# Kernel tuning notes

Hardware: AMD Instinct MI355X
Metric: run time of the kernel (lower is better)

Reference implementation:

```python
import jax, jax.numpy as jnp
import numpy as np

NUM_RELATIONS = 65
NUM_GRAPHS = 1600


def rgcn_conv(x, src, dst, etype, W, Wroot, b):
    """PyG RGCNConv: per-relation mean aggregation + root transform + bias.
    out_i = x_i @ Wroot + b + sum_r mean_{j in N_r(i)} (x_j) @ W_r
    (mean-then-transform == transform-then-mean since W_r is linear).
    """
    N = x.shape[0]
    x_src = x[src]  # [E, in]
    etype_f = etype

    def body(acc, rW):
        r, Wr = rW
        m = (etype_f == r).astype(x.dtype)[:, None]  # [E,1]
        s = jax.ops.segment_sum(x_src * m, dst, num_segments=N)   # [N,in]
        cnt = jax.ops.segment_sum(m, dst, num_segments=N)          # [N,1]
        mean = s / jnp.maximum(cnt, 1.0)
        return acc + mean @ Wr, None

    acc0 = x @ Wroot + b
    out, _ = jax.lax.scan(body, acc0, (jnp.arange(W.shape[0]), W))
    return out


def setup_inputs() -> dict:
    key = jax.random.key(0)
    ks = jax.random.split(key, 20)
    N, E, F, H, M = 50000, 200000, 128, 256, 64
    x = jax.random.normal(ks[0], (N, F), dtype=jnp.float32)
    edge_index = jax.random.randint(ks[1], (2, E), 0, N, dtype=jnp.int64)
    edge_type = jax.random.randint(ks[2], (E,), 0, NUM_RELATIONS, dtype=jnp.int64)
    batch = jnp.sort(jax.random.randint(ks[3], (N,), 0, NUM_GRAPHS, dtype=jnp.int64))

    def glorot(k, shape):
        fan_in = shape[-2] if len(shape) > 1 else shape[-1]
        return jax.random.normal(k, shape, dtype=jnp.float32) / np.sqrt(fan_in)

    W1 = glorot(ks[4], (NUM_RELATIONS, F, H))
    root1 = glorot(ks[5], (F, H))
    b1 = jnp.zeros((H,), jnp.float32)
    W2 = glorot(ks[6], (NUM_RELATIONS, H, H))
    root2 = glorot(ks[7], (H, H))
    b2 = jnp.zeros((H,), jnp.float32)
    ws_w = glorot(ks[8], (H, 1))
    ws_b = jnp.zeros((1,), jnp.float32)
    m1w = glorot(ks[9], (H, M)); m1b = jnp.zeros((M,), jnp.float32)
    m2w = glorot(ks[10], (M, M)); m2b = jnp.zeros((M,), jnp.float32)
    m3w = glorot(ks[11], (M, M)); m3b = jnp.zeros((M,), jnp.float32)
    ow = glorot(ks[12], (M, 1)); ob = jnp.zeros((1,), jnp.float32)
    return {"x": x, "edge_index": edge_index, "edge_type": edge_type, "batch": batch,
            "W1": W1, "root1": root1, "b1": b1, "W2": W2, "root2": root2, "b2": b2,
            "ws_w": ws_w, "ws_b": ws_b, "m1w": m1w, "m1b": m1b, "m2w": m2w,
            "m2b": m2b, "m3w": m3w, "m3b": m3b, "ow": ow, "ob": ob}


def reference(x, edge_index, edge_type, batch, W1, root1, b1, W2, root2, b2,
              ws_w, ws_b, m1w, m1b, m2w, m2b, m3w, m3b, ow, ob):
    N = x.shape[0]
    # add_self_loops(fill_value=0): append self edges with relation 0
    loop = jnp.arange(N, dtype=edge_index.dtype)
    src = jnp.concatenate([edge_index[0], loop])
    dst = jnp.concatenate([edge_index[1], loop])
    et = jnp.concatenate([edge_type, jnp.zeros((N,), edge_type.dtype)])

    h = jax.nn.relu(rgcn_conv(x, src, dst, et, W1, root1, b1))   # dropout: eval
    h = jax.nn.relu(rgcn_conv(h, src, dst, et, W2, root2, b2))

    # WeightedSum pooling
    w = jax.nn.sigmoid(h @ ws_w + ws_b)                          # [N,1]
    emb = jax.ops.segment_sum(w * h, batch, num_segments=NUM_GRAPHS)  # [G,H]

    # MLP (3 layers; eval batch-norm with default stats ~ identity)
    z = jax.nn.relu(emb @ m1w + m1b)
    z = jax.nn.relu(z @ m2w + m2b)
    z = z @ m3w + m3b
    return z @ ow + ob
```

## Files before the change

kernel.cpp:

```cpp
#include <hip/hip_runtime.h>
#include <math.h>

#define N_NODES 50000
#define E_REAL  200000
#define E_MEAN  250000
#define NREL    65
#define HDIM    256
#define NGRAPH  1600
#define NB_R    ((E_REAL + 255) / 256)
#define NB_CNT  ((E_MEAN + 255) / 256)
#define TOT_HIST (NREL * NB_R)
#define MB      64
#define MAX_PB  3264

typedef __attribute__((ext_vector_type(8))) short short8;
typedef __attribute__((ext_vector_type(4))) float floatx4;
typedef const __attribute__((address_space(1))) void GPtr;
typedef __attribute__((address_space(3))) void LPtr;

__device__ __forceinline__ unsigned short f2bf(float f) {
    unsigned int u = __float_as_uint(f);
    unsigned int r = u + 0x7FFFu + ((u >> 16) & 1u);
    return (unsigned short)(r >> 16);
}
__device__ __forceinline__ float bf2f(unsigned short u) {
    return __uint_as_float(((unsigned int)u) << 16);
}

__device__ __forceinline__ void gl_lds16(const unsigned short* g, unsigned short* l) {
    __builtin_amdgcn_global_load_lds((GPtr*)g,
        (LPtr*)(unsigned int)(unsigned long long)(void*)l, 16, 0, 0);
}

__global__ void count_kernel(const int* __restrict__ src, const int* __restrict__ dst,
                             const int* __restrict__ et, int* __restrict__ cnt,
                             int* __restrict__ blockHist, int* __restrict__ cntD) {
    __shared__ int lhist[NREL];
    int t = threadIdx.x;
    if (t < NREL) lhist[t] = 0;
    __syncthreads();
    int e = blockIdx.x * 256 + t;
    if (e < E_REAL) {
        int d = dst[e], r = et[e];
        atomicAdd(&cnt[d * NREL + r], 1);
        atomicAdd(&cntD[d], 1);
        atomicAdd(&lhist[r], 1);
    } else if (e < E_MEAN) {
        atomicAdd(&cnt[(e - E_REAL) * NREL], 1);
    }
    __syncthreads();
    if (t < NREL && blockIdx.x < NB_R) blockHist[t * NB_R + blockIdx.x] = lhist[t];
}

__global__ void scan_part(const int* __restrict__ in, int* __restrict__ psum, int n) {
    __shared__ int red[1024];
    int t = threadIdx.x;
    int g = blockIdx.x * 1024 + t;
    red[t] = (g < n) ? in[g] : 0;
    __syncthreads();
    for (int off = 512; off >= 1; off >>= 1) {
        if (t < off) red[t] += red[t + off];
        __syncthreads();
    }
    if (t == 0) psum[blockIdx.x] = red[0];
}

__global__ void scan_apply(const int* __restrict__ in, const int* __restrict__ psum,
                           int* __restrict__ out, int* __restrict__ out2, int n) {
    __shared__ int sums[1024];
    __shared__ int soff;
    int t = threadIdx.x;
    int b = blockIdx.x;
    int g = b * 1024 + t;
    if (t < 64) {
        int v = (t < b) ? psum[t] : 0;
        for (int off = 32; off >= 1; off >>= 1) v += __shfl_down(v, off, 64);
        if (t == 0) soff = v;
    }
    int v = (g < n) ? in[g] : 0;
    sums[t] = v;
    __syncthreads();
    for (int off = 1; off < 1024; off <<= 1) {
        int u = (t >= off) ? sums[t - off] : 0;
        __syncthreads();
        sums[t] += u;
        __syncthreads();
    }
    if (g < n) {
        int excl = soff + sums[t] - v;
        out[g] = excl;
        if (out2) out2[g] = excl;
    }
}

__global__ void meta_kernel(const int* __restrict__ baseArr,
                            int* __restrict__ relStart, int* __restrict__ relTot,
                            int* __restrict__ pBlockStart, int* __restrict__ relOfBlock,
                            int* __restrict__ npb) {
    __shared__ int sStart[NREL + 1];
    __shared__ int sPB[NREL + 1];
    int t = threadIdx.x;
    if (t < NREL) sStart[t] = baseArr[t * NB_R];
    if (t == 0) sStart[NREL] = E_REAL;
    __syncthreads();
    if (t < NREL) {
        relStart[t] = sStart[t];
        relTot[t] = sStart[t + 1] - sStart[t];
    }
    if (t == 0) {
        int a2 = 0;
        for (int r = 0; r < NREL; ++r) {
            sPB[r] = a2;
            int tot = sStart[r + 1] - sStart[r];
            a2 += (tot + MB - 1) / MB;
        }
        sPB[NREL] = a2;
        npb[0] = a2;
    }
    __syncthreads();
    if (t < NREL) pBlockStart[t] = sPB[t];
    int NPB = sPB[NREL];
    for (int b = t; b < NPB; b += 1024) {
        int lo = 0, hi = NREL - 1;
        while (lo < hi) { int mid = (lo + hi + 1) >> 1; if (sPB[mid] <= b) lo = mid; else hi = mid - 1; }
        relOfBlock[b] = lo;
    }
}

__global__ void scatter_sorted(const int* __restrict__ src, const int* __restrict__ dst,
                               const int* __restrict__ et, const int* __restrict__ base,
                               int* __restrict__ perm, int* __restrict__ cursorD,
                               int* __restrict__ qofp) {
    __shared__ int lhist[NREL];
    int t = threadIdx.x;
    int b = blockIdx.x;
    if (t < NREL) lhist[t] = 0;
    __syncthreads();
    int e = b * 256 + t;
    if (e < E_REAL) {
        int d = dst[e], r = et[e];
        int local = atomicAdd(&lhist[r], 1);
        int p = base[r * NB_R + b] + local;
        perm[p] = e;
        int q = atomicAdd(&cursorD[d], 1);
        qofp[p] = q;
    }
}

__global__ void cvt_rows(const float* __restrict__ in, unsigned short* __restrict__ out,
                         int nchunk, int relu) {
    int i = blockIdx.x * 256 + threadIdx.x;
    if (i >= nchunk) return;
    const float4* p = (const float4*)in + (size_t)i * 2;
    float4 a = p[0], b = p[1];
    float v[8] = {a.x, a.y, a.z, a.w, b.x, b.y, b.z, b.w};
    short8 o;
#pragma unroll
    for (int j = 0; j < 8; ++j) {
        float f = relu ? fmaxf(v[j], 0.f) : v[j];
        o[j] = (short)f2bf(f);
    }
    ((short8*)out)[i] = o;
}

__global__ void cvt_wT(const float* __restrict__ W, unsigned short* __restrict__ out,
                       int R, int K, int N) {
    int kc8 = K / 8;
    int total = R * N * kc8;
    int i = blockIdx.x * 256 + threadIdx.x;
    if (i >= total) return;
    int kc = i % kc8;
    int tmp = i / kc8;
    int n = tmp % N;
    int r = tmp / N;
    const float* src = W + ((size_t)r * K + kc * 8) * N + n;
    short8 o;
#pragma unroll
    for (int j = 0; j < 8; ++j) o[j] = (short)f2bf(src[(size_t)j * N]);
    ((short8*)out)[i] = o;
}

template<int K>
__device__ __forceinline__ void gemm_pass(const unsigned short* __restrict__ Bp,
                                          const unsigned short* lds,
                                          int lrow, int lk, floatx4 (&acc)[4][4]) {
    constexpr int KS = K / 32;
    short8 bb[3][4];
#pragma unroll
    for (int nf = 0; nf < 4; ++nf)
        bb[0][nf] = *(const short8*)(Bp + (size_t)(nf * 16 + lrow) * K + lk * 8);
#pragma unroll
    for (int nf = 0; nf < 4; ++nf)
        bb[1][nf] = *(const short8*)(Bp + (size_t)(nf * 16 + lrow) * K + 32 + lk * 8);
#pragma unroll
    for (int ks = 0; ks < KS; ++ks) {
        short8 a[4];
#pragma unroll
        for (int mf = 0; mf < 4; ++mf) {
            int row = mf * 16 + lrow;
            int c = (ks * 4 + lk) ^ (row & 7);
            a[mf] = *(const short8*)((const char*)lds + row * (K * 2) + c * 16);
        }
        if (ks + 2 < KS) {
#pragma unroll
            for (int nf = 0; nf < 4; ++nf)
                bb[(ks + 2) % 3][nf] = *(const short8*)(Bp + (size_t)(nf * 16 + lrow) * K + (ks + 2) * 32 + lk * 8);
        }
#pragma unroll
        for (int mf = 0; mf < 4; ++mf)
#pragma unroll
            for (int nf = 0; nf < 4; ++nf)
                acc[mf][nf] = __builtin_amdgcn_mfma_f32_16x16x32_bf16(a[mf], bb[ks % 3][nf], acc[mf][nf], 0, 0, 0);
    }
}

template<int K, bool EDGE>
__device__ __forceinline__ void stage_A(const unsigned short* __restrict__ A,
                                        unsigned short* lds, const int* ssrc,
                                        int rowbase, int t) {
    constexpr int CH = K / 8;
#pragma unroll
    for (int i = 0; i < (MB * CH) / 256; ++i) {
        int q = i * 256 + t;
        int row = q / CH, sl = q % CH;
        int srow;
        if constexpr (EDGE) srow = ssrc[row];
        else { srow = rowbase + row; if (srow >= N_NODES) srow = N_NODES - 1; }
        int cg = sl ^ (row & 7);
        gl_lds16(A + (size_t)srow * K + cg * 8, lds + q * 8);
    }
}

template<int K, int MODE>
__global__ __launch_bounds__(256) void mfma_gemm(
    const unsigned short* __restrict__ A,
    const unsigned short* __restrict__ B,
    const unsigned short* __restrict__ Bself,
    const float* __restrict__ bias,
    float* __restrict__ outF,
    unsigned short* __restrict__ outB,
    const int* __restrict__ perm, const int* __restrict__ srcA,
    const int* __restrict__ dstA, const int* __restrict__ etA,
    const int* __restrict__ cnt,
    const int* __restrict__ relOfBlock, const int* __restrict__ pBlockStart,
    const int* __restrict__ relStart, const int* __restrict__ relTot,
    const int* __restrict__ npb, const int* __restrict__ qofp)
{
    constexpr bool EDGE = (MODE == 1 || MODE == 3);
    __shared__ __align__(16) unsigned short lds[MB * HDIM];
    __shared__ int ssrc[MB];
    __shared__ int sdst[MB];
    __shared__ int sqd[MB];
    __shared__ float sw[MB];
    int t = threadIdx.x;
    int b = blockIdx.x;
    int rel = 0, rowbase = 0, jb = 0, rs = 0, nval = MB;
    if constexpr (EDGE) {
        if (b >= npb[0]) return;
        rel = relOfBlock[b];
        jb = b - pBlockStart[rel];
        rs = relStart[rel];
        nval = relTot[rel] - jb * MB; if (nval > MB) nval = MB;
        if (t < MB) {
            int s = 0, d = 0, qd = 0; float w = 0.f;
            if (t < nval) {
                int p = rs + jb * MB + t;
                int e = perm[p];
                s = srcA[e]; d = dstA[e];
                w = 1.0f / (float)cnt[d * NREL + rel];
                if constexpr (MODE == 3) qd = qofp[p];
            }
            ssrc[t] = s; sdst[t] = d; sw[t] = w; sqd[t] = qd;
        }
        __syncthreads();
    } else {
        rowbase = b * MB;
        if (t < MB) {
            int srow = rowbase + t; if (srow >= N_NODES) srow = N_NODES - 1;
            sw[t] = 1.0f / (float)cnt[srow * NREL];
        }
    }
    stage_A<K, EDGE>(A, lds, ssrc, rowbase, t);
    __syncthreads();

    int wave = t >> 6, lane = t & 63;
    int n0 = wave * 64;
    int lrow = lane & 15;
    int lk = lane >> 4;
    floatx4 acc[4][4];
#pragma unroll
    for (int mf = 0; mf < 4; ++mf)
#pragma unroll
        for (int nf = 0; nf < 4; ++nf) acc[mf][nf] = (floatx4)0.f;

    if constexpr (EDGE) {
        gemm_pass<K>(B + ((size_t)rel * HDIM + n0) * K, lds, lrow, lk, acc);
    } else {
        gemm_pass<K>(Bself + (size_t)n0 * K, lds, lrow, lk, acc);
#pragma unroll
        for (int mf = 0; mf < 4; ++mf) {
            int mbase = mf * 16 + lk * 4;
#pragma unroll
            for (int i = 0; i < 4; ++i) {
                float w = sw[mbase + i];
#pragma unroll
                for (int nf = 0; nf < 4; ++nf) acc[mf][nf][i] *= w;
            }
        }
        gemm_pass<K>(B + (size_t)n0 * K, lds, lrow, lk, acc);
    }

    if constexpr (MODE == 1) {
#pragma unroll
        for (int mf = 0; mf < 4; ++mf) {
            int mbase = mf * 16 + lk * 4;
#pragma unroll
            for (int i = 0; i < 4; ++i) {
                int mm = mbase + i;
                float w = sw[mm];
                if (w != 0.f) {
                    int drow = sdst[mm];
#pragma unroll
                    for (int nf = 0; nf < 4; ++nf) {
                        int col = n0 + nf * 16 + lrow;
                        atomicAdd(&outF[(size_t)drow * HDIM + col], acc[mf][nf][i] * w);
                    }
                }
            }
        }
    } else if constexpr (MODE == 0) {
        float bv[4];
#pragma unroll
        for (int nf = 0; nf < 4; ++nf) bv[nf] = bias[n0 + nf * 16 + lrow];
#pragma unroll
        for (int mf = 0; mf < 4; ++mf) {
            int mbase = mf * 16 + lk * 4;
#pragma unroll
            for (int i = 0; i < 4; ++i) {
                int mm = rowbase + mbase + i;
                if (mm < N_NODES) {
#pragma unroll
                    for (int nf = 0; nf < 4; ++nf) {
                        int col = n0 + nf * 16 + lrow;
                        outF[(size_t)mm * HDIM + col] = acc[mf][nf][i] + bv[nf];
                    }
                }
            }
        }
    } else {
        float bv[4];
        if constexpr (MODE == 2) {
#pragma unroll
            for (int nf = 0; nf < 4; ++nf) bv[nf] = bias[n0 + nf * 16 + lrow];
        }
        __syncthreads();
#pragma unroll
        for (int mf = 0; mf < 4; ++mf) {
            int mbase = mf * 16 + lk * 4;
#pragma unroll
            for (int i = 0; i < 4; ++i) {
                int row = mbase + i;
                float w = (MODE == 3) ? sw[row] : 0.f;
#pragma unroll
                for (int nf = 0; nf < 4; ++nf) {
                    int col = n0 + nf * 16 + lrow;
                    float v = acc[mf][nf][i];
                    if constexpr (MODE == 3) v *= w;
                    else v += bv[nf];
                    lds[row * HDIM + col] = f2bf(v);
                }
            }
        }
        __syncthreads();
        if constexpr (MODE == 3) {
            for (int q = t; q < nval * 32; q += 256) {
                int row = q >> 5, c = q & 31;
                *(uint4*)(outB + (size_t)sqd[row] * HDIM + c * 8) = *(const uint4*)(lds + row * HDIM + c * 8);
            }
        } else {
            int limit = N_NODES - rowbase; if (limit > MB) limit = MB;
            for (int q = t; q < limit * 32; q += 256) {
                int row = q >> 5, c = q & 31;
                *(uint4*)(outB + ((size_t)rowbase + row) * HDIM + c * 8) = *(const uint4*)(lds + row * HDIM + c * 8);
            }
        }
    }
}

__global__ __launch_bounds__(256) void reduce_kernel(
    const unsigned short* __restrict__ hinit, const unsigned short* __restrict__ msg,
    const int* __restrict__ startD, const int* __restrict__ cntD,
    unsigned short* __restrict__ hout)
{
    int t = threadIdx.x;
    int lane = t & 63;
    int d = blockIdx.x * 4 + (t >> 6);
    if (d >= N_NODES) return;
    int s0 = startD[d], n = cntD[d];
    ushort4 hv = *(const ushort4*)(hinit + (size_t)d * HDIM + lane * 4);
    float v0 = bf2f(hv.x), v1 = bf2f(hv.y), v2 = bf2f(hv.z), v3 = bf2f(hv.w);
    const unsigned short* mp = msg + (size_t)s0 * HDIM + lane * 4;
#pragma unroll 4
    for (int q = 0; q < n; ++q) {
        ushort4 m = *(const ushort4*)(mp + (size_t)q * HDIM);
        v0 += bf2f(m.x); v1 += bf2f(m.y); v2 += bf2f(m.z); v3 += bf2f(m.w);
    }
    ushort4 o;
    o.x = f2bf(fmaxf(v0, 0.f)); o.y = f2bf(fmaxf(v1, 0.f));
    o.z = f2bf(fmaxf(v2, 0.f)); o.w = f2bf(fmaxf(v3, 0.f));
    *(ushort4*)(hout + (size_t)d * HDIM + lane * 4) = o;
}

__global__ __launch_bounds__(256) void pool_graph(
    const unsigned short* __restrict__ h, const int* __restrict__ batch,
    const float* __restrict__ wsw, const float* __restrict__ wsb,
    float* __restrict__ emb)
{
    int g = blockIdx.x;
    int t = threadIdx.x;
    __shared__ int slo, shi;
    __shared__ float sacc[4][HDIM];
    if (t == 0) {
        int lo = 0, hi = N_NODES;
        while (lo < hi) { int m = (lo + hi) >> 1; if (batch[m] < g) lo = m + 1; else hi = m; }
        slo = lo;
        int lo2 = lo, hi2 = N_NODES;
        while (lo2 < hi2) { int m = (lo2 + hi2) >> 1; if (batch[m] < g + 1) lo2 = m + 1; else hi2 = m; }
        shi = lo2;
    }
    __syncthreads();
    int wave = t >> 6, lane = t & 63;
    float4 wv = *(const float4*)(wsw + lane * 4);
    float wb = wsb[0];
    float a0 = 0.f, a1 = 0.f, a2 = 0.f, a3 = 0.f;
    for (int i = slo + wave; i < shi; i += 4) {
        ushort4 hv = *(const ushort4*)(h + (size_t)i * HDIM + lane * 4);
        float v0 = bf2f(hv.x), v1 = bf2f(hv.y), v2 = bf2f(hv.z), v3 = bf2f(hv.w);
        float pp = v0 * wv.x + v1 * wv.y + v2 * wv.z + v3 * wv.w;
        for (int off = 32; off >= 1; off >>= 1) pp += __shfl_down(pp, off, 64);
        float tot = __shfl(pp, 0, 64);
        float sig = 1.0f / (1.0f + expf(-(tot + wb)));
        a0 += sig * v0; a1 += sig * v1; a2 += sig * v2; a3 += sig * v3;
    }
    sacc[wave][lane * 4 + 0] = a0; sacc[wave][lane * 4 + 1] = a1;
    sacc[wave][lane * 4 + 2] = a2; sacc[wave][lane * 4 + 3] = a3;
    __syncthreads();
    emb[(size_t)g * HDIM + t] = sacc[0][t] + sacc[1][t] + sacc[2][t] + sacc[3][t];
}

__global__ void pool_kernel(const float* __restrict__ h, const int* __restrict__ batch,
                            const float* __restrict__ wsw, const float* __restrict__ wsb,
                            float* __restrict__ emb) {
    int i = blockIdx.x;
    int t = threadIdx.x;
    float v = fmaxf(h[(size_t)i * HDIM + t], 0.f);
    float p = v * wsw[t];
    for (int off = 32; off >= 1; off >>= 1) p += __shfl_down(p, off, 64);
    __shared__ float red[4];
    __shared__ float ssig;
    if ((t & 63) == 0) red[t >> 6] = p;
    __syncthreads();
    if (t == 0) {
        float s = red[0] + red[1] + red[2] + red[3] + wsb[0];
        ssig = 1.0f / (1.0f + expf(-s));
    }
    __syncthreads();
    atomicAdd(&emb[(size_t)batch[i] * HDIM + t], ssig * v);
}

__global__ void mlp_kernel(const float* __restrict__ emb,
                           const float* __restrict__ m1w, const float* __restrict__ m1b,
                           const float* __restrict__ m2w, const float* __restrict__ m2b,
                           const float* __restrict__ m3w, const float* __restrict__ m3b,
                           const float* __restrict__ ow,  const float* __restrict__ ob,
                           float* __restrict__ out) {
    int g = blockIdx.x;
    int t = threadIdx.x;
    __shared__ float e[HDIM];
    __shared__ float z1[64], z2[64];
    for (int idx = t; idx < HDIM; idx += 64) e[idx] = emb[(size_t)g * HDIM + idx];
    __syncthreads();
    float a = m1b[t];
    for (int k = 0; k < HDIM; ++k) a += e[k] * m1w[k * 64 + t];
    z1[t] = fmaxf(a, 0.f);
    __syncthreads();
    a = m2b[t];
    for (int k = 0; k < 64; ++k) a += z1[k] * m2w[k * 64 + t];
    z2[t] = fmaxf(a, 0.f);
    __syncthreads();
    a = m3b[t];
    for (int k = 0; k < 64; ++k) a += z2[k] * m3w[k * 64 + t];
    float p = a * ow[t];
    for (int off = 32; off >= 1; off >>= 1) p += __shfl_down(p, off, 64);
    if (t == 0) out[g] = p + ob[0];
}

extern "C" void kernel_launch(void* const* d_in, const int* in_sizes, int n_in,
                              void* d_out, int out_size, void* d_ws, size_t ws_size,
                              hipStream_t stream) {
    const float* x     = (const float*)d_in[0];
    const int*   ei    = (const int*)d_in[1];
    const int*   src   = ei;
    const int*   dst   = ei + E_REAL;
    const int*   et    = (const int*)d_in[2];
    const int*   batch = (const int*)d_in[3];
    const float* W1    = (const float*)d_in[4];
    const float* root1 = (const float*)d_in[5];
    const float* b1    = (const float*)d_in[6];
    const float* W2    = (const float*)d_in[7];
    const float* root2 = (const float*)d_in[8];
    const float* b2    = (const float*)d_in[9];
    const float* wsw   = (const float*)d_in[10];
    const float* wsb   = (const float*)d_in[11];
    const float* m1w   = (const float*)d_in[12];
    const float* m1b   = (const float*)d_in[13];
    const float* m2w   = (const float*)d_in[14];
    const float* m2b   = (const float*)d_in[15];
    const float* m3w   = (const float*)d_in[16];
    const float* m3b   = (const float*)d_in[17];
    const float* ow    = (const float*)d_in[18];
    const float* ob    = (const float*)d_in[19];

    char* ws = (char*)d_ws;
    size_t off = 0;
    auto alloc = [&](size_t bytes) {
        void* p = ws + off;
        off = (off + bytes + 255) & ~(size_t)255;
        return p;
    };
    int*   cnt       = (int*)alloc((size_t)N_NODES * NREL * 4);
    int*   blockHist = (int*)alloc((size_t)TOT_HIST * 4);
    int*   baseArr   = (int*)alloc((size_t)TOT_HIST * 4);
    int*   perm      = (int*)alloc((size_t)E_REAL * 4);
    int*   relStartA = (int*)alloc(NREL * 4);
    int*   relTotA   = (int*)alloc(NREL * 4);
    int*   pbStartA  = (int*)alloc(NREL * 4);
    int*   relOfBlk  = (int*)alloc(MAX_PB * 4);
    int*   npb       = (int*)alloc(4);
    int*   psumA     = (int*)alloc(64 * 4);
    int*   psumB     = (int*)alloc(64 * 4);
    unsigned short* xb  = (unsigned short*)alloc((size_t)N_NODES * 128 * 2);
    unsigned short* w1b = (unsigned short*)alloc((size_t)NREL * 256 * 128 * 2);
    unsigned short* w2b = (unsigned short*)alloc((size_t)NREL * 256 * 256 * 2);
    unsigned short* r1b = (unsigned short*)alloc((size_t)256 * 128 * 2);
    unsigned short* r2b = (unsigned short*)alloc((size_t)256 * 256 * 2);
    unsigned short* h1b = (unsigned short*)alloc((size_t)N_NODES * HDIM * 2);
    float* emb = (float*)alloc((size_t)NGRAPH * HDIM * 4);
    size_t off_common = off;

    unsigned short* hinit = (unsigned short*)alloc((size_t)N_NODES * HDIM * 2);
    unsigned short* msg   = (unsigned short*)alloc((size_t)E_REAL * HDIM * 2);
    int* qofp    = (int*)alloc((size_t)E_REAL * 4);
    int* cntD    = (int*)alloc((size_t)N_NODES * 4);
    int* startD  = (int*)alloc((size_t)N_NODES * 4);
    int* cursorD = (int*)alloc((size_t)N_NODES * 4);
    size_t need_fast = off;

    float* hf = nullptr;
    bool fast = (ws_size >= need_fast);
    if (!fast) {
        off = off_common;
        hf = (float*)alloc((size_t)N_NODES * HDIM * 4);
        char* hh = (char*)hf;
        qofp    = (int*)hh;                                 hh += (size_t)E_REAL * 4;
        cntD    = (int*)hh;                                 hh += (size_t)N_NODES * 4;
        startD  = (int*)hh;                                 hh += (size_t)N_NODES * 4;
        cursorD = (int*)hh;
        hinit = h1b;
        msg = h1b;
    }

    hipMemsetAsync(cnt, 0, (size_t)N_NODES * NREL * 4, stream);
    hipMemsetAsync(cntD, 0, (size_t)N_NODES * 4, stream);
    hipMemsetAsync(emb, 0, (size_t)NGRAPH * HDIM * 4, stream);

    count_kernel<<<NB_CNT, 256, 0, stream>>>(src, dst, et, cnt, blockHist, cntD);
    scan_part<<<64, 1024, 0, stream>>>(blockHist, psumA, TOT_HIST);
    scan_apply<<<64, 1024, 0, stream>>>(blockHist, psumA, baseArr, nullptr, TOT_HIST);
    meta_kernel<<<1, 1024, 0, stream>>>(baseArr, relStartA, relTotA, pbStartA, relOfBlk, npb);
    scan_part<<<64, 1024, 0, stream>>>(cntD, psumB, N_NODES);
    scan_apply<<<64, 1024, 0, stream>>>(cntD, psumB, startD, cursorD, N_NODES);
    scatter_sorted<<<NB_R, 256, 0, stream>>>(src, dst, et, baseArr, perm, cursorD, qofp);

    cvt_rows<<<(N_NODES * 128 / 8 + 255) / 256, 256, 0, stream>>>(x, xb, N_NODES * 128 / 8, 0);
    cvt_wT<<<(NREL * 256 * 16 + 255) / 256, 256, 0, stream>>>(W1, w1b, NREL, 128, 256);
    cvt_wT<<<(NREL * 256 * 32 + 255) / 256, 256, 0, stream>>>(W2, w2b, NREL, 256, 256);
    cvt_wT<<<(256 * 16 + 255) / 256, 256, 0, stream>>>(root1, r1b, 1, 128, 256);
    cvt_wT<<<(256 * 32 + 255) / 256, 256, 0, stream>>>(root2, r2b, 1, 256, 256);

    const int grid_init = (N_NODES + MB - 1) / MB;

    if (fast) {
        mfma_gemm<128, 2><<<grid_init, 256, 0, stream>>>(xb, r1b, w1b, b1, nullptr, hinit,
            nullptr, nullptr, nullptr, nullptr, cnt, nullptr, nullptr, nullptr, nullptr, nullptr, nullptr);
        mfma_gemm<128, 3><<<MAX_PB, 256, 0, stream>>>(xb, w1b, nullptr, nullptr, nullptr, msg,
            perm, src, dst, et, cnt, relOfBlk, pbStartA, relStartA, relTotA, npb, qofp);
        reduce_kernel<<<N_NODES / 4, 256, 0, stream>>>(hinit, msg, startD, cntD, h1b);
        mfma_gemm<256, 2><<<grid_init, 256, 0, stream>>>(h1b, r2b, w2b, b2, nullptr, hinit,
            nullptr, nullptr, nullptr, nullptr, cnt, nullptr, nullptr, nullptr, nullptr, nullptr, nullptr);
        mfma_gemm<256, 3><<<MAX_PB, 256, 0, stream>>>(h1b, w2b, nullptr, nullptr, nullptr, msg,
            perm, src, dst, et, cnt, relOfBlk, pbStartA, relStartA, relTotA, npb, qofp);
        reduce_kernel<<<N_NODES / 4, 256, 0, stream>>>(hinit, msg, startD, cntD, h1b);
        pool_graph<<<NGRAPH, 256, 0, stream>>>(h1b, batch, wsw, wsb, emb);
    } else {
        mfma_gemm<128, 0><<<grid_init, 256, 0, stream>>>(xb, r1b, w1b, b1, hf, nullptr,
            nullptr, nullptr, nullptr, nullptr, cnt, nullptr, nullptr, nullptr, nullptr, nullptr, nullptr);
        mfma_gemm<128, 1><<<MAX_PB, 256, 0, stream>>>(xb, w1b, nullptr, nullptr, hf, nullptr,
            perm, src, dst, et, cnt, relOfBlk, pbStartA, relStartA, relTotA, npb, nullptr);
        cvt_rows<<<(N_NODES * HDIM / 8 + 255) / 256, 256, 0, stream>>>(hf, h1b, N_NODES * HDIM / 8, 1);
        mfma_gemm<256, 0><<<grid_init, 256, 0, stream>>>(h1b, r2b, w2b, b2, hf, nullptr,
            nullptr, nullptr, nullptr, nullptr, cnt, nullptr, nullptr, nullptr, nullptr, nullptr, nullptr);
        mfma_gemm<256, 1><<<MAX_PB, 256, 0, stream>>>(h1b, w2b, nullptr, nullptr, hf, nullptr,
            perm, src, dst, et, cnt, relOfBlk, pbStartA, relStartA, relTotA, npb, nullptr);
        pool_kernel<<<N_NODES, 256, 0, stream>>>(hf, batch, wsw, wsb, emb);
    }
    mlp_kernel<<<NGRAPH, 64, 0, stream>>>(emb, m1w, m1b, m2w, m2b, m3w, m3b, ow, ob, (float*)d_out);
}
```

Baseline: 378.2 us.

## Process two 64-edge tiles per block in dedicated edge message kernel

```diff
diff --git a/kernel.cpp b/kernel.cpp
--- a/kernel.cpp
+++ b/kernel.cpp
@@ -12,6 +12,7 @@
 #define TOT_HIST (NREL * NB_R)
 #define MB      64
 #define MAX_PB  3264
+#define MAX_PB2 1700
 
 typedef __attribute__((ext_vector_type(8))) short short8;
 typedef __attribute__((ext_vector_type(4))) float floatx4;
@@ -96,9 +97,12 @@
 __global__ void meta_kernel(const int* __restrict__ baseArr,
                             int* __restrict__ relStart, int* __restrict__ relTot,
                             int* __restrict__ pBlockStart, int* __restrict__ relOfBlock,
-                            int* __restrict__ npb) {
+                            int* __restrict__ npb,
+                            int* __restrict__ pbs2, int* __restrict__ relOfBlk2,
+                            int* __restrict__ npb2) {
     __shared__ int sStart[NREL + 1];
     __shared__ int sPB[NREL + 1];
+    __shared__ int sPB2[NREL + 1];
     int t = threadIdx.x;
     if (t < NREL) sStart[t] = baseArr[t * NB_R];
     if (t == 0) sStart[NREL] = E_REAL;
@@ -108,22 +112,30 @@
         relTot[t] = sStart[t + 1] - sStart[t];
     }
     if (t == 0) {
-        int a2 = 0;
+        int a2 = 0, a3 = 0;
         for (int r = 0; r < NREL; ++r) {
             sPB[r] = a2;
+            sPB2[r] = a3;
             int tot = sStart[r + 1] - sStart[r];
             a2 += (tot + MB - 1) / MB;
-        }
-        sPB[NREL] = a2;
-        npb[0] = a2;
-    }
-    __syncthreads();
-    if (t < NREL) pBlockStart[t] = sPB[t];
+            a3 += (tot + 127) / 128;
+        }
+        sPB[NREL] = a2;  npb[0] = a2;
+        sPB2[NREL] = a3; npb2[0] = a3;
+    }
+    __syncthreads();
+    if (t < NREL) { pBlockStart[t] = sPB[t]; pbs2[t] = sPB2[t]; }
     int NPB = sPB[NREL];
     for (int b = t; b < NPB; b += 1024) {
         int lo = 0, hi = NREL - 1;
         while (lo < hi) { int mid = (lo + hi + 1) >> 1; if (sPB[mid] <= b) lo = mid; else hi = mid - 1; }
         relOfBlock[b] = lo;
+    }
+    int NPB2 = sPB2[NREL];
+    for (int b = t; b < NPB2; b += 1024) {
+        int lo = 0, hi = NREL - 1;
+        while (lo < hi) { int mid = (lo + hi + 1) >> 1; if (sPB2[mid] <= b) lo = mid; else hi = mid - 1; }
+        relOfBlk2[b] = lo;
     }
 }
 
@@ -228,6 +240,113 @@
         else { srow = rowbase + row; if (srow >= N_NODES) srow = N_NODES - 1; }
         int cg = sl ^ (row & 7);
         gl_lds16(A + (size_t)srow * K + cg * 8, lds + q * 8);
+    }
+}
+
+template<int K>
+__global__ __launch_bounds__(256) void edge_msg(
+    const unsigned short* __restrict__ A,
+    const unsigned short* __restrict__ B,
+    unsigned short* __restrict__ outB,
+    const int* __restrict__ perm, const int* __restrict__ srcA,
+    const int* __restrict__ dstA, const int* __restrict__ cnt,
+    const int* __restrict__ relOfBlk2, const int* __restrict__ pbs2,
+    const int* __restrict__ relStart, const int* __restrict__ relTot,
+    const int* __restrict__ npb2, const int* __restrict__ qofp)
+{
+    __shared__ __align__(16) unsigned short lds[32768];
+    __shared__ int ssrc[128];
+    __shared__ int sqd[128];
+    __shared__ float sw[128];
+    int t = threadIdx.x;
+    int b = blockIdx.x;
+    if (b >= npb2[0]) return;
+    int rel = relOfBlk2[b];
+    int jb = b - pbs2[rel];
+    int rs = relStart[rel];
+    int tot = relTot[rel];
+    int base = jb * 128;
+    int rem = tot - base;
+    int nv0 = rem > 64 ? 64 : rem;
+    int nv1 = rem - 64; if (nv1 < 0) nv1 = 0; if (nv1 > 64) nv1 = 64;
+    if (t < 128) {
+        int s = 0, qd = 0; float w = 0.f;
+        if (t < rem) {
+            int p = rs + base + t;
+            int e = perm[p];
+            s = srcA[e];
+            int d = dstA[e];
+            w = 1.0f / (float)cnt[d * NREL + rel];
+            qd = qofp[p];
+        }
+        ssrc[t] = s; sqd[t] = qd; sw[t] = w;
+    }
+    __syncthreads();
+
+    unsigned short* buf0 = lds;
+    unsigned short* buf1 = lds + MB * K;
+    unsigned short* pack = (K == 256) ? lds : lds + 2 * MB * K;
+
+    stage_A<K, true>(A, buf0, ssrc, 0, t);
+    __syncthreads();
+    if (nv1 > 0) stage_A<K, true>(A, buf1, ssrc + 64, 0, t);
+
+    int wave = t >> 6, lane = t & 63;
+    int n0 = wave * 64;
+    int lrow = lane & 15, lk = lane >> 4;
+    const unsigned short* Bp = B + ((size_t)rel * HDIM + n0) * K;
+
+    {
+        floatx4 acc[4][4];
+#pragma unroll
+        for (int mf = 0; mf < 4; ++mf)
+#pragma unroll
+            for (int nf = 0; nf < 4; ++nf) acc[mf][nf] = (floatx4)0.f;
+        gemm_pass<K>(Bp, buf0, lrow, lk, acc);
+        __syncthreads();
+#pragma unroll
+        for (int mf = 0; mf < 4; ++mf) {
+            int mbase = mf * 16 + lk * 4;
+#pragma unroll
+            for (int i = 0; i < 4; ++i) {
+                int row = mbase + i;
+                float w = sw[row];
+#pragma unroll
+                for (int nf = 0; nf < 4; ++nf)
+                    pack[row * HDIM + n0 + nf * 16 + lrow] = f2bf(acc[mf][nf][i] * w);
+            }
+        }
+        __syncthreads();
+        for (int q = t; q < nv0 * 32; q += 256) {
+            int row = q >> 5, c = q & 31;
+            *(uint4*)(outB + (size_t)sqd[row] * HDIM + c * 8) = *(const uint4*)(pack + row * HDIM + c * 8);
+        }
+    }
+    if (nv1 > 0) {
+        __syncthreads();
+        floatx4 acc[4][4];
+#pragma unroll
+        for (int mf = 0; mf < 4; ++mf)
+#pragma unroll
+            for (int nf = 0; nf < 4; ++nf) acc[mf][nf] = (floatx4)0.f;
+        gemm_pass<K>(Bp, buf1, lrow, lk, acc);
+#pragma unroll
+        for (int mf = 0; mf < 4; ++mf) {
+            int mbase = mf * 16 + lk * 4;
+#pragma unroll
+            for (int i = 0; i < 4; ++i) {
+                int row = mbase + i;
+                float w = sw[64 + row];
+#pragma unroll
+                for (int nf = 0; nf < 4; ++nf)
+                    pack[row * HDIM + n0 + nf * 16 + lrow] = f2bf(acc[mf][nf][i] * w);
+            }
+        }
+        __syncthreads();
+        for (int q = t; q < nv1 * 32; q += 256) {
+            int row = q >> 5, c = q & 31;
+            *(uint4*)(outB + (size_t)sqd[64 + row] * HDIM + c * 8) = *(const uint4*)(pack + row * HDIM + c * 8);
+        }
     }
 }
 
@@ -244,13 +363,12 @@
     const int* __restrict__ cnt,
     const int* __restrict__ relOfBlock, const int* __restrict__ pBlockStart,
     const int* __restrict__ relStart, const int* __restrict__ relTot,
-    const int* __restrict__ npb, const int* __restrict__ qofp)
+    const int* __restrict__ npb)
 {
-    constexpr bool EDGE = (MODE == 1 || MODE == 3);
+    constexpr bool EDGE = (MODE == 1);
     __shared__ __align__(16) unsigned short lds[MB * HDIM];
     __shared__ int ssrc[MB];
     __shared__ int sdst[MB];
-    __shared__ int sqd[MB];
     __shared__ float sw[MB];
     int t = threadIdx.x;
     int b = blockIdx.x;
@@ -262,15 +380,14 @@
         rs = relStart[rel];
         nval = relTot[rel] - jb * MB; if (nval > MB) nval = MB;
         if (t < MB) {
-            int s = 0, d = 0, qd = 0; float w = 0.f;
+            int s = 0, d = 0; float w = 0.f;
             if (t < nval) {
                 int p = rs + jb * MB + t;
                 int e = perm[p];
                 s = srcA[e]; d = dstA[e];
                 w = 1.0f / (float)cnt[d * NREL + rel];
-                if constexpr (MODE == 3) qd = qofp[p];
             }
-            ssrc[t] = s; sdst[t] = d; sw[t] = w; sqd[t] = qd;
+            ssrc[t] = s; sdst[t] = d; sw[t] = w;
         }
         __syncthreads();
     } else {
@@ -349,10 +466,8 @@
         }
     } else {
         float bv[4];
-        if constexpr (MODE == 2) {
-#pragma unroll
-            for (int nf = 0; nf < 4; ++nf) bv[nf] = bias[n0 + nf * 16 + lrow];
-        }
+#pragma unroll
+        for (int nf = 0; nf < 4; ++nf) bv[nf] = bias[n0 + nf * 16 + lrow];
         __syncthreads();
 #pragma unroll
         for (int mf = 0; mf < 4; ++mf) {
@@ -360,29 +475,18 @@
 #pragma unroll
             for (int i = 0; i < 4; ++i) {
                 int row = mbase + i;
-                float w = (MODE == 3) ? sw[row] : 0.f;
 #pragma unroll
                 for (int nf = 0; nf < 4; ++nf) {
                     int col = n0 + nf * 16 + lrow;
-                    float v = acc[mf][nf][i];
-                    if constexpr (MODE == 3) v *= w;
-                    else v += bv[nf];
-                    lds[row * HDIM + col] = f2bf(v);
+                    lds[row * HDIM + col] = f2bf(acc[mf][nf][i] + bv[nf]);
                 }
             }
         }
         __syncthreads();
-        if constexpr (MODE == 3) {
-            for (int q = t; q < nval * 32; q += 256) {
-                int row = q >> 5, c = q & 31;
-                *(uint4*)(outB + (size_t)sqd[row] * HDIM + c * 8) = *(const uint4*)(lds + row * HDIM + c * 8);
-            }
-        } else {
-            int limit = N_NODES - rowbase; if (limit > MB) limit = MB;
-            for (int q = t; q < limit * 32; q += 256) {
-                int row = q >> 5, c = q & 31;
-                *(uint4*)(outB + ((size_t)rowbase + row) * HDIM + c * 8) = *(const uint4*)(lds + row * HDIM + c * 8);
-            }
+        int limit = N_NODES - rowbase; if (limit > MB) limit = MB;
+        for (int q = t; q < limit * 32; q += 256) {
+            int row = q >> 5, c = q & 31;
+            *(uint4*)(outB + ((size_t)rowbase + row) * HDIM + c * 8) = *(const uint4*)(lds + row * HDIM + c * 8);
         }
     }
 }
@@ -537,6 +641,9 @@
     int*   pbStartA  = (int*)alloc(NREL * 4);
     int*   relOfBlk  = (int*)alloc(MAX_PB * 4);
     int*   npb       = (int*)alloc(4);
+    int*   pbs2A     = (int*)alloc(NREL * 4);
+    int*   relOfBlk2 = (int*)alloc(MAX_PB2 * 4);
+    int*   npb2      = (int*)alloc(4);
     int*   psumA     = (int*)alloc(64 * 4);
     int*   psumB     = (int*)alloc(64 * 4);
     unsigned short* xb  = (unsigned short*)alloc((size_t)N_NODES * 128 * 2);
@@ -577,7 +684,8 @@
     count_kernel<<<NB_CNT, 256, 0, stream>>>(src, dst, et, cnt, blockHist, cntD);
     scan_part<<<64, 1024, 0, stream>>>(blockHist, psumA, TOT_HIST);
     scan_apply<<<64, 1024, 0, stream>>>(blockHist, psumA, baseArr, nullptr, TOT_HIST);
-    meta_kernel<<<1, 1024, 0, stream>>>(baseArr, relStartA, relTotA, pbStartA, relOfBlk, npb);
+    meta_kernel<<<1, 1024, 0, stream>>>(baseArr, relStartA, relTotA, pbStartA, relOfBlk,
+                                        npb, pbs2A, relOfBlk2, npb2);
     scan_part<<<64, 1024, 0, stream>>>(cntD, psumB, N_NODES);
     scan_apply<<<64, 1024, 0, stream>>>(cntD, psumB, startD, cursorD, N_NODES);
     scatter_sorted<<<NB_R, 256, 0, stream>>>(src, dst, et, baseArr, perm, cursorD, qofp);
@@ -592,26 +700,26 @@
 
     if (fast) {
         mfma_gemm<128, 2><<<grid_init, 256, 0, stream>>>(xb, r1b, w1b, b1, nullptr, hinit,
-            nullptr, nullptr, nullptr, nullptr, cnt, nullptr, nullptr, nullptr, nullptr, nullptr, nullptr);
-        mfma_gemm<128, 3><<<MAX_PB, 256, 0, stream>>>(xb, w1b, nullptr, nullptr, nullptr, msg,
-            perm, src, dst, et, cnt, relOfBlk, pbStartA, relStartA, relTotA, npb, qofp);
+            nullptr, nullptr, nullptr, nullptr, cnt, nullptr, nullptr, nullptr, nullptr, nullptr);
+        edge_msg<128><<<MAX_PB2, 256, 0, stream>>>(xb, w1b, msg,
+            perm, src, dst, cnt, relOfBlk2, pbs2A, relStartA, relTotA, npb2, qofp);
         reduce_kernel<<<N_NODES / 4, 256, 0, stream>>>(hinit, msg, startD, cntD, h1b);
         mfma_gemm<256, 2><<<grid_init, 256, 0, stream>>>(h1b, r2b, w2b, b2, nullptr, hinit,
-            nullptr, nullptr, nullptr, nullptr, cnt, nullptr, nullptr, nullptr, nullptr, nullptr, nullptr);
-        mfma_gemm<256, 3><<<MAX_PB, 256, 0, stream>>>(h1b, w2b, nullptr, nullptr, nullptr, msg,
-            perm, src, dst, et, cnt, relOfBlk, pbStartA, relStartA, relTotA, npb, qofp);
+            nullptr, nullptr, nullptr, nullptr, cnt, nullptr, nullptr, nullptr, nullptr, nullptr);
+        edge_msg<256><<<MAX_PB2, 256, 0, stream>>>(h1b, w2b, msg,
+            perm, src, dst, cnt, relOfBlk2, pbs2A, relStartA, relTotA, npb2, qofp);
         reduce_kernel<<<N_NODES / 4, 256, 0, stream>>>(hinit, msg, startD, cntD, h1b);
         pool_graph<<<NGRAPH, 256, 0, stream>>>(h1b, batch, wsw, wsb, emb);
     } else {
         mfma_gemm<128, 0><<<grid_init, 256, 0, stream>>>(xb, r1b, w1b, b1, hf, nullptr,
-            nullptr, nullptr, nullptr, nullptr, cnt, nullptr, nullptr, nullptr, nullptr, nullptr, nullptr);
+            nullptr, nullptr, nullptr, nullptr, cnt, nullptr, nullptr, nullptr, nullptr, nullptr);
         mfma_gemm<128, 1><<<MAX_PB, 256, 0, stream>>>(xb, w1b, nullptr, nullptr, hf, nullptr,
-            perm, src, dst, et, cnt, relOfBlk, pbStartA, relStartA, relTotA, npb, nullptr);
+            perm, src, dst, et, cnt, relOfBlk, pbStartA, relStartA, relTotA, npb);
         cvt_rows<<<(N_NODES * HDIM / 8 + 255) / 256, 256, 0, stream>>>(hf, h1b, N_NODES * HDIM / 8, 1);
         mfma_gemm<256, 0><<<grid_init, 256, 0, stream>>>(h1b, r2b, w2b, b2, hf, nullptr,
-            nullptr, nullptr, nullptr, nullptr, cnt, nullptr, nullptr, nullptr, nullptr, nullptr, nullptr);
+            nullptr, nullptr, nullptr, nullptr, cnt, nullptr, nullptr, nullptr, nullptr, nullptr);
         mfma_gemm<256, 1><<<MAX_PB, 256, 0, stream>>>(h1b, w2b, nullptr, nullptr, hf, nullptr,
-            perm, src, dst, et, cnt, relOfBlk, pbStartA, relStartA, relTotA, npb, nullptr);
+            perm, src, dst, et, cnt, relOfBlk, pbStartA, relStartA, relTotA, npb);
         pool_kernel<<<N_NODES, 256, 0, stream>>>(hf, batch, wsw, wsb, emb);
     }
     mlp_kernel<<<NGRAPH, 64, 0, stream>>>(emb, m1w, m1b, m2w, m2b, m3w, m3b, ow, ob, (float*)d_out);
```

After: 382.7 us. No clear change (+1.2%).

## Fuse root and edge GEMMs into one interleaved launch; merge conversion kernels

Applied to the files above, without the earlier changes.

```diff
diff --git a/kernel.cpp b/kernel.cpp
--- a/kernel.cpp
+++ b/kernel.cpp
@@ -12,6 +12,8 @@
 #define TOT_HIST (NREL * NB_R)
 #define MB      64
 #define MAX_PB  3264
+#define GRID_I  ((N_NODES + MB - 1) / MB)
+#define GRID_F  4000
 
 typedef __attribute__((ext_vector_type(8))) short short8;
 typedef __attribute__((ext_vector_type(4))) float floatx4;
@@ -147,10 +149,9 @@
     }
 }
 
-__global__ void cvt_rows(const float* __restrict__ in, unsigned short* __restrict__ out,
-                         int nchunk, int relu) {
-    int i = blockIdx.x * 256 + threadIdx.x;
-    if (i >= nchunk) return;
+__device__ __forceinline__ void cvt_row_chunk(const float* __restrict__ in,
+                                              unsigned short* __restrict__ out,
+                                              int i, int relu) {
     const float4* p = (const float4*)in + (size_t)i * 2;
     float4 a = p[0], b = p[1];
     float v[8] = {a.x, a.y, a.z, a.w, b.x, b.y, b.z, b.w};
@@ -162,13 +163,10 @@
     }
     ((short8*)out)[i] = o;
 }
-
-__global__ void cvt_wT(const float* __restrict__ W, unsigned short* __restrict__ out,
-                       int R, int K, int N) {
+__device__ __forceinline__ void cvt_wT_chunk(const float* __restrict__ W,
+                                             unsigned short* __restrict__ out,
+                                             int i, int K, int N) {
     int kc8 = K / 8;
-    int total = R * N * kc8;
-    int i = blockIdx.x * 256 + threadIdx.x;
-    if (i >= total) return;
     int kc = i % kc8;
     int tmp = i / kc8;
     int n = tmp % N;
@@ -178,6 +176,37 @@
 #pragma unroll
     for (int j = 0; j < 8; ++j) o[j] = (short)f2bf(src[(size_t)j * N]);
     ((short8*)out)[i] = o;
+}
+
+__global__ void cvt_rows(const float* __restrict__ in, unsigned short* __restrict__ out,
+                         int nchunk, int relu) {
+    int i = blockIdx.x * 256 + threadIdx.x;
+    if (i >= nchunk) return;
+    cvt_row_chunk(in, out, i, relu);
+}
+
+#define CVT_NX  (N_NODES * 128 / 8)
+#define CVT_W1  (NREL * 256 * 16)
+#define CVT_W2  (NREL * 256 * 32)
+#define CVT_R1  (256 * 16)
+#define CVT_R2  (256 * 32)
+#define CVT_TOT (CVT_NX + CVT_W1 + CVT_W2 + CVT_R1 + CVT_R2)
+__global__ void cvt_all(const float* __restrict__ x, const float* __restrict__ W1,
+                        const float* __restrict__ W2, const float* __restrict__ root1,
+                        const float* __restrict__ root2,
+                        unsigned short* __restrict__ xb, unsigned short* __restrict__ w1b,
+                        unsigned short* __restrict__ w2b, unsigned short* __restrict__ r1b,
+                        unsigned short* __restrict__ r2b) {
+    int i = blockIdx.x * 256 + threadIdx.x;
+    if (i < CVT_NX) { cvt_row_chunk(x, xb, i, 0); return; }
+    i -= CVT_NX;
+    if (i < CVT_W1) { cvt_wT_chunk(W1, w1b, i, 128, 256); return; }
+    i -= CVT_W1;
+    if (i < CVT_W2) { cvt_wT_chunk(W2, w2b, i, 256, 256); return; }
+    i -= CVT_W2;
+    if (i < CVT_R1) { cvt_wT_chunk(root1, r1b, i, 128, 256); return; }
+    i -= CVT_R1;
+    if (i < CVT_R2) { cvt_wT_chunk(root2, r2b, i, 256, 256); return; }
 }
 
 template<int K>
@@ -231,6 +260,133 @@
     }
 }
 
+template<int K>
+__global__ __launch_bounds__(256) void fused_gemm(
+    const unsigned short* __restrict__ A,
+    const unsigned short* __restrict__ B,
+    const unsigned short* __restrict__ Broot,
+    const float* __restrict__ bias,
+    unsigned short* __restrict__ hinitOut,
+    unsigned short* __restrict__ msgOut,
+    const int* __restrict__ perm, const int* __restrict__ srcA,
+    const int* __restrict__ dstA, const int* __restrict__ cnt,
+    const int* __restrict__ relOfBlock, const int* __restrict__ pBlockStart,
+    const int* __restrict__ relStart, const int* __restrict__ relTot,
+    const int* __restrict__ npb, const int* __restrict__ qofp)
+{
+    __shared__ __align__(16) unsigned short lds[MB * HDIM];
+    __shared__ int ssrc[MB];
+    __shared__ int sqd[MB];
+    __shared__ float sw[MB];
+    int t = threadIdx.x;
+    int b = blockIdx.x;
+    int r5 = b % 5;
+    bool isInit = (r5 == 4);
+    int wave = t >> 6, lane = t & 63;
+    int n0 = wave * 64;
+    int lrow = lane & 15, lk = lane >> 4;
+
+    if (isInit) {
+        int i = b / 5;
+        if (i >= GRID_I) return;
+        int rowbase = i * MB;
+        if (t < MB) {
+            int srow = rowbase + t; if (srow >= N_NODES) srow = N_NODES - 1;
+            sw[t] = 1.0f / (float)cnt[srow * NREL];
+        }
+        stage_A<K, false>(A, lds, nullptr, rowbase, t);
+        __syncthreads();
+
+        floatx4 acc[4][4];
+#pragma unroll
+        for (int mf = 0; mf < 4; ++mf)
+#pragma unroll
+            for (int nf = 0; nf < 4; ++nf) acc[mf][nf] = (floatx4)0.f;
+        gemm_pass<K>(B + (size_t)n0 * K, lds, lrow, lk, acc);
+#pragma unroll
+        for (int mf = 0; mf < 4; ++mf) {
+            int mbase = mf * 16 + lk * 4;
+#pragma unroll
+            for (int i2 = 0; i2 < 4; ++i2) {
+                float w = sw[mbase + i2];
+#pragma unroll
+                for (int nf = 0; nf < 4; ++nf) acc[mf][nf][i2] *= w;
+            }
+        }
+        gemm_pass<K>(Broot + (size_t)n0 * K, lds, lrow, lk, acc);
+
+        float bv[4];
+#pragma unroll
+        for (int nf = 0; nf < 4; ++nf) bv[nf] = bias[n0 + nf * 16 + lrow];
+        __syncthreads();
+#pragma unroll
+        for (int mf = 0; mf < 4; ++mf) {
+            int mbase = mf * 16 + lk * 4;
+#pragma unroll
+            for (int i2 = 0; i2 < 4; ++i2) {
+                int row = mbase + i2;
+#pragma unroll
+                for (int nf = 0; nf < 4; ++nf)
+                    lds[row * HDIM + n0 + nf * 16 + lrow] = f2bf(acc[mf][nf][i2] + bv[nf]);
+            }
+        }
+        __syncthreads();
+        int limit = N_NODES - rowbase; if (limit > MB) limit = MB;
+        for (int q = t; q < limit * 32; q += 256) {
+            int row = q >> 5, c = q & 31;
+            *(uint4*)(hinitOut + ((size_t)rowbase + row) * HDIM + c * 8) = *(const uint4*)(lds + row * HDIM + c * 8);
+        }
+    } else {
+        int e = (b / 5) * 4 + r5;
+        if (e >= npb[0]) return;
+        int rel = relOfBlock[e];
+        int jb = e - pBlockStart[rel];
+        int rs = relStart[rel];
+        int nval = relTot[rel] - jb * MB; if (nval > MB) nval = MB;
+        if (t < MB) {
+            int s = 0, qd = 0; float w = 0.f;
+            if (t < nval) {
+                int p = rs + jb * MB + t;
+                int ed = perm[p];
+                s = srcA[ed];
+                int d = dstA[ed];
+                w = 1.0f / (float)cnt[d * NREL + rel];
+                qd = qofp[p];
+            }
+            ssrc[t] = s; sqd[t] = qd; sw[t] = w;
+        }
+        __syncthreads();
+        stage_A<K, true>(A, lds, ssrc, 0, t);
+        __syncthreads();
+
+        floatx4 acc[4][4];
+#pragma unroll
+        for (int mf = 0; mf < 4; ++mf)
+#pragma unroll
+            for (int nf = 0; nf < 4; ++nf) acc[mf][nf] = (floatx4)0.f;
+        gemm_pass<K>(B + ((size_t)rel * HDIM + n0) * K, lds, lrow, lk, acc);
+
+        __syncthreads();
+#pragma unroll
+        for (int mf = 0; mf < 4; ++mf) {
+            int mbase = mf * 16 + lk * 4;
+#pragma unroll
+            for (int i2 = 0; i2 < 4; ++i2) {
+                int row = mbase + i2;
+                float w = sw[row];
+#pragma unroll
+                for (int nf = 0; nf < 4; ++nf)
+                    lds[row * HDIM + n0 + nf * 16 + lrow] = f2bf(acc[mf][nf][i2] * w);
+            }
+        }
+        __syncthreads();
+        for (int q = t; q < nval * 32; q += 256) {
+            int row = q >> 5, c = q & 31;
+            *(uint4*)(msgOut + (size_t)sqd[row] * HDIM + c * 8) = *(const uint4*)(lds + row * HDIM + c * 8);
+        }
+    }
+}
+
 template<int K, int MODE>
 __global__ __launch_bounds__(256) void mfma_gemm(
     const unsigned short* __restrict__ A,
@@ -238,19 +394,16 @@
     const unsigned short* __restrict__ Bself,
     const float* __restrict__ bias,
     float* __restrict__ outF,
-    unsigned short* __restrict__ outB,
     const int* __restrict__ perm, const int* __restrict__ srcA,
-    const int* __restrict__ dstA, const int* __restrict__ etA,
-    const int* __restrict__ cnt,
+    const int* __restrict__ dstA, const int* __restrict__ cnt,
     const int* __restrict__ relOfBlock, const int* __restrict__ pBlockStart,
     const int* __restrict__ relStart, const int* __restrict__ relTot,
-    const int* __restrict__ npb, const int* __restrict__ qofp)
+    const int* __restrict__ npb)
 {
-    constexpr bool EDGE = (MODE == 1 || MODE == 3);
+    constexpr bool EDGE = (MODE == 1);
     __shared__ __align__(16) unsigned short lds[MB * HDIM];
     __shared__ int ssrc[MB];
     __shared__ int sdst[MB];
-    __shared__ int sqd[MB];
     __shared__ float sw[MB];
     int t = threadIdx.x;
     int b = blockIdx.x;
@@ -262,15 +415,14 @@
         rs = relStart[rel];
         nval = relTot[rel] - jb * MB; if (nval > MB) nval = MB;
         if (t < MB) {
-            int s = 0, d = 0, qd = 0; float w = 0.f;
+            int s = 0, d = 0; float w = 0.f;
             if (t < nval) {
                 int p = rs + jb * MB + t;
                 int e = perm[p];
                 s = srcA[e]; d = dstA[e];
                 w = 1.0f / (float)cnt[d * NREL + rel];
-                if constexpr (MODE == 3) qd = qofp[p];
             }
-            ssrc[t] = s; sdst[t] = d; sw[t] = w; sqd[t] = qd;
+            ssrc[t] = s; sdst[t] = d; sw[t] = w;
         }
         __syncthreads();
     } else {
@@ -328,7 +480,7 @@
                 }
             }
         }
-    } else if constexpr (MODE == 0) {
+    } else {
         float bv[4];
 #pragma unroll
         for (int nf = 0; nf < 4; ++nf) bv[nf] = bias[n0 + nf * 16 + lrow];
@@ -345,43 +497,6 @@
                         outF[(size_t)mm * HDIM + col] = acc[mf][nf][i] + bv[nf];
                     }
                 }
-            }
-        }
-    } else {
-        float bv[4];
-        if constexpr (MODE == 2) {
-#pragma unroll
-            for (int nf = 0; nf < 4; ++nf) bv[nf] = bias[n0 + nf * 16 + lrow];
-        }
-        __syncthreads();
-#pragma unroll
-        for (int mf = 0; mf < 4; ++mf) {
-            int mbase = mf * 16 + lk * 4;
-#pragma unroll
-            for (int i = 0; i < 4; ++i) {
-                int row = mbase + i;
-                float w = (MODE == 3) ? sw[row] : 0.f;
-#pragma unroll
-                for (int nf = 0; nf < 4; ++nf) {
-                    int col = n0 + nf * 16 + lrow;
-                    float v = acc[mf][nf][i];
-                    if constexpr (MODE == 3) v *= w;
-                    else v += bv[nf];
-                    lds[row * HDIM + col] = f2bf(v);
-                }
-            }
-        }
-        __syncthreads();
-        if constexpr (MODE == 3) {
-            for (int q = t; q < nval * 32; q += 256) {
-                int row = q >> 5, c = q & 31;
-                *(uint4*)(outB + (size_t)sqd[row] * HDIM + c * 8) = *(const uint4*)(lds + row * HDIM + c * 8);
-            }
-        } else {
-            int limit = N_NODES - rowbase; if (limit > MB) limit = MB;
-            for (int q = t; q < limit * 32; q += 256) {
-                int row = q >> 5, c = q & 31;
-                *(uint4*)(outB + ((size_t)rowbase + row) * HDIM + c * 8) = *(const uint4*)(lds + row * HDIM + c * 8);
             }
         }
     }
@@ -582,36 +697,27 @@
     scan_apply<<<64, 1024, 0, stream>>>(cntD, psumB, startD, cursorD, N_NODES);
     scatter_sorted<<<NB_R, 256, 0, stream>>>(src, dst, et, baseArr, perm, cursorD, qofp);
 
-    cvt_rows<<<(N_NODES * 128 / 8 + 255) / 256, 256, 0, stream>>>(x, xb, N_NODES * 128 / 8, 0);
-    cvt_wT<<<(NREL * 256 * 16 + 255) / 256, 256, 0, stream>>>(W1, w1b, NREL, 128, 256);
-    cvt_wT<<<(NREL * 256 * 32 + 255) / 256, 256, 0, stream>>>(W2, w2b, NREL, 256, 256);
-    cvt_wT<<<(256 * 16 + 255) / 256, 256, 0, stream>>>(root1, r1b, 1, 128, 256);
-    cvt_wT<<<(256 * 32 + 255) / 256, 256, 0, stream>>>(root2, r2b, 1, 256, 256);
-
-    const int grid_init = (N_NODES + MB - 1) / MB;
+    cvt_all<<<(CVT_TOT + 255) / 256, 256, 0, stream>>>(x, W1, W2, root1, root2,
+                                                       xb, w1b, w2b, r1b, r2b);
 
     if (fast) {
-        mfma_gemm<128, 2><<<grid_init, 256, 0, stream>>>(xb, r1b, w1b, b1, nullptr, hinit,
-            nullptr, nullptr, nullptr, nullptr, cnt, nullptr, nullptr, nullptr, nullptr, nullptr, nullptr);
-        mfma_gemm<128, 3><<<MAX_PB, 256, 0, stream>>>(xb, w1b, nullptr, nullptr, nullptr, msg,
-            perm, src, dst, et, cnt, relOfBlk, pbStartA, relStartA, relTotA, npb, qofp);
+        fused_gemm<128><<<GRID_F, 256, 0, stream>>>(xb, w1b, r1b, b1, hinit, msg,
+            perm, src, dst, cnt, relOfBlk, pbStartA, relStartA, relTotA, npb, qofp);
         reduce_kernel<<<N_NODES / 4, 256, 0, stream>>>(hinit, msg, startD, cntD, h1b);
-        mfma_gemm<256, 2><<<grid_init, 256, 0, stream>>>(h1b, r2b, w2b, b2, nullptr, hinit,
-            nullptr, nullptr, nullptr, nullptr, cnt, nullptr, nullptr, nullptr, nullptr, nullptr, nullptr);
-        mfma_gemm<256, 3><<<MAX_PB, 256, 0, stream>>>(h1b, w2b, nullptr, nullptr, nullptr, msg,
-            perm, src, dst, et, cnt, relOfBlk, pbStartA, relStartA, relTotA, npb, qofp);
+        fused_gemm<256><<<GRID_F, 256, 0, stream>>>(h1b, w2b, r2b, b2, hinit, msg,
+            perm, src, dst, cnt, relOfBlk, pbStartA, relStartA, relTotA, npb, qofp);
         reduce_kernel<<<N_NODES / 4, 256, 0, stream>>>(hinit, msg, startD, cntD, h1b);
         pool_graph<<<NGRAPH, 256, 0, stream>>>(h1b, batch, wsw, wsb, emb);
     } else {
-        mfma_gemm<128, 0><<<grid_init, 256, 0, stream>>>(xb, r1b, w1b, b1, hf, nullptr,
-            nullptr, nullptr, nullptr, nullptr, cnt, nullptr, nullptr, nullptr, nullptr, nullptr, nullptr);
-        mfma_gemm<128, 1><<<MAX_PB, 256, 0, stream>>>(xb, w1b, nullptr, nullptr, hf, nullptr,
-            perm, src, dst, et, cnt, relOfBlk, pbStartA, relStartA, relTotA, npb, nullptr);
+        mfma_gemm<128, 0><<<GRID_I, 256, 0, stream>>>(xb, r1b, w1b, b1, hf,
+            nullptr, nullptr, nullptr, cnt, nullptr, nullptr, nullptr, nullptr, nullptr);
+        mfma_gemm<128, 1><<<MAX_PB, 256, 0, stream>>>(xb, w1b, nullptr, nullptr, hf,
+            perm, src, dst, cnt, relOfBlk, pbStartA, relStartA, relTotA, npb);
         cvt_rows<<<(N_NODES * HDIM / 8 + 255) / 256, 256, 0, stream>>>(hf, h1b, N_NODES * HDIM / 8, 1);
-        mfma_gemm<256, 0><<<grid_init, 256, 0, stream>>>(h1b, r2b, w2b, b2, hf, nullptr,
-            nullptr, nullptr, nullptr, nullptr, cnt, nullptr, nullptr, nullptr, nullptr, nullptr, nullptr);
-        mfma_gemm<256, 1><<<MAX_PB, 256, 0, stream>>>(h1b, w2b, nullptr, nullptr, hf, nullptr,
-            perm, src, dst, et, cnt, relOfBlk, pbStartA, relStartA, relTotA, npb, nullptr);
+        mfma_gemm<256, 0><<<GRID_I, 256, 0, stream>>>(h1b, r2b, w2b, b2, hf,
+            nullptr, nullptr, nullptr, cnt, nullptr, nullptr, nullptr, nullptr, nullptr);
+        mfma_gemm<256, 1><<<MAX_PB, 256, 0, stream>>>(h1b, w2b, nullptr, nullptr, hf,
+            perm, src, dst, cnt, relOfBlk, pbStartA, relStartA, relTotA, npb);
         pool_kernel<<<N_NODES, 256, 0, stream>>>(hf, batch, wsw, wsb, emb);
     }
     mlp_kernel<<<NGRAPH, 64, 0, stream>>>(emb, m1w, m1b, m2w, m2b, m3w, m3b, ow, ob, (float*)d_out);
```

New measurement: 361.3 us. -4.4%, faster.
